# Performance work log

Measured on AMD Instinct MI355X. Metric: run time of the kernel, lower is better.

## Reference

```python
import jax, jax.numpy as jnp
import numpy as np

INPUT_DIM, HIDDEN, EVENT_DIM = 64, 256, 32
B, T = 128, 1024


def setup_inputs() -> dict:
    key = jax.random.key(0)
    ks = jax.random.split(key, 20)
    s = 0.02
    return {
        "x": jax.random.normal(ks[0], (B, T, INPUT_DIM), jnp.float32),
        "events": jax.random.normal(ks[1], (B, T, EVENT_DIM), jnp.float32),
        "time_distances": jax.random.uniform(ks[2], (B, T), jnp.float32),
        # input projection
        "W_proj": s * jax.random.normal(ks[3], (INPUT_DIM, HIDDEN), jnp.float32),
        "b_proj": jnp.zeros((HIDDEN,), jnp.float32),
        # custom LSTM cell (input = projected_x of size HIDDEN)
        "W_ih": s * jax.random.normal(ks[4], (HIDDEN, 4 * HIDDEN), jnp.float32),
        "W_hh": s * jax.random.normal(ks[5], (HIDDEN, 4 * HIDDEN), jnp.float32),
        "b_lstm": jnp.zeros((4 * HIDDEN,), jnp.float32),
        # market-state gate from raw x
        "W_mk": s * jax.random.normal(ks[6], (INPUT_DIM, HIDDEN), jnp.float32),
        "b_mk": jnp.zeros((HIDDEN,), jnp.float32),
        # event processor
        "W_e": s * jax.random.normal(ks[7], (EVENT_DIM, HIDDEN), jnp.float32),
        "b_e": jnp.zeros((HIDDEN,), jnp.float32),
        "W_hg": s * jax.random.normal(ks[8], (HIDDEN, HIDDEN), jnp.float32),
        "b_hg": jnp.zeros((HIDDEN,), jnp.float32),
        "decay": jnp.asarray(0.5, jnp.float32),
        # predictor MLP (dropout is eval-mode identity)
        "W_p1": s * jax.random.normal(ks[9], (HIDDEN, HIDDEN // 2), jnp.float32),
        "b_p1": jnp.zeros((HIDDEN // 2,), jnp.float32),
        "W_p2": s * jax.random.normal(ks[10], (HIDDEN // 2, 1), jnp.float32),
        "b_p2": jnp.zeros((1,), jnp.float32),
    }


def _tmdo(x):
    # temporal first difference and Laplacian (second difference), zero-padded to [B,T,D]
    d1 = jnp.concatenate([jnp.zeros_like(x[:, :1]), x[:, 1:] - x[:, :-1]], axis=1)
    lap = jnp.concatenate(
        [jnp.zeros_like(x[:, :1]),
         x[:, 2:] - 2.0 * x[:, 1:-1] + x[:, :-2],
         jnp.zeros_like(x[:, :1])], axis=1)
    return d1, lap


def reference(x, events, time_distances, W_proj, b_proj, W_ih, W_hh, b_lstm,
              W_mk, b_mk, W_e, b_e, W_hg, b_hg, decay, W_p1, b_p1, W_p2, b_p2):
    bsz, seq_len, _ = x.shape
    H = W_proj.shape[1]
    tmdo_features, lap_features = _tmdo(x)

    h0 = jnp.zeros((bsz, H), x.dtype)
    c0 = jnp.zeros((bsz, H), x.dtype)

    def step(carry, inp):
        h, c = carry
        xt, et, dt = inp  # [B,D_in], [B,E], [B]
        px = xt @ W_proj + b_proj                                  # input_proj
        # event processor: embedded event * hidden gate * time decay
        e = jnp.tanh(et @ W_e + b_e)
        gate = jax.nn.sigmoid(h @ W_hg + b_hg)
        impact = e * gate * jnp.exp(-jax.nn.softplus(decay) * dt[:, None])
        # custom LSTM cell with market gate from raw x and event injection
        gates = px @ W_ih + h @ W_hh + b_lstm
        i_g, f_g, g_g, o_g = jnp.split(gates, 4, axis=-1)
        mk = jax.nn.sigmoid(xt @ W_mk + b_mk)
        c_new = jax.nn.sigmoid(f_g) * c + jax.nn.sigmoid(i_g) * jnp.tanh(g_g) \
                + mk * jnp.tanh(impact)
        h_new = jax.nn.sigmoid(o_g) * jnp.tanh(c_new)
        # predictor (exact GELU like torch nn.GELU; dropout = identity in eval)
        pred = jax.nn.gelu(h_new @ W_p1 + b_p1, approximate=False) @ W_p2 + b_p2
        return (h_new, c_new), (pred, h_new)

    xs = (jnp.swapaxes(x, 0, 1), jnp.swapaxes(events, 0, 1),
          jnp.swapaxes(time_distances, 0, 1))
    _, (preds, feats) = jax.lax.scan(step, (h0, c0), xs)
    predictions = jnp.swapaxes(preds, 0, 1)  # [B,T,1]
    features = jnp.swapaxes(feats, 0, 1)     # [B,T,H]
    return predictions, features, tmdo_features
```

## Files before the change

kernel.cpp:

```cpp
#include <hip/hip_runtime.h>
#include <hip/hip_bf16.h>
#include <hip/hip_fp16.h>
#include <math.h>

#define BB 128
#define TT 1024
#define DIN 64
#define HH 256
#define EE 32
#define BT (BB * TT)

typedef unsigned int uint;
typedef unsigned char uchar;
typedef _Float16 half2v __attribute__((ext_vector_type(2)));

__device__ __forceinline__ int dot4(uint a, uint b, int c) {
  return __builtin_amdgcn_sdot4((int)a, (int)b, c, false);
}
__device__ __forceinline__ uint pkh(float a, float b) {
  return __builtin_bit_cast(uint, __builtin_amdgcn_cvt_pkrtz(a, b));
}
__device__ __forceinline__ half2v uph(uint u) { return __builtin_bit_cast(half2v, u); }
__device__ __forceinline__ float fdot2u(uint a, uint b, float c) {
  return __builtin_amdgcn_fdot2(uph(a), uph(b), c, false);
}
#define IDPP(v, c) __builtin_amdgcn_mov_dpp((v), (c), 0xF, 0xF, true)
__device__ __forceinline__ int qsum(int v) {
  v += IDPP(v, 0xB1);
  v += IDPP(v, 0x4E);
  return v;
}
__device__ __forceinline__ float rcp_f(float x) { return __builtin_amdgcn_rcpf(x); }
__device__ __forceinline__ float sigm(float x) { return rcp_f(1.0f + __expf(-x)); }
__device__ __forceinline__ float tanh_f(float x) {
  return 1.0f - 2.0f * rcp_f(__expf(2.0f * x) + 1.0f);
}

__global__ void fold_f32(const float* __restrict__ Wproj, const float* __restrict__ Wih,
                         float* __restrict__ Wfold) {
  int idx = blockIdx.x * blockDim.x + threadIdx.x;
  if (idx >= 64 * 1024) return;
  int d = idx >> 10, n = idx & 1023;
  float a = 0.f;
  for (int k = 0; k < 256; ++k) a += Wproj[d * 256 + k] * Wih[k * 1024 + n];
  Wfold[d * 1024 + n] = a;
}

__global__ void bfold_kernel(const float* __restrict__ bproj, const float* __restrict__ Wih,
                             const float* __restrict__ blstm, float* __restrict__ bfold) {
  int n = blockIdx.x * blockDim.x + threadIdx.x;
  if (n >= 1024) return;
  float a = blstm[n];
  for (int k = 0; k < 256; ++k) a += bproj[k] * Wih[k * 1024 + n];
  bfold[n] = a;
}

__global__ __launch_bounds__(1024) void quant_all(
    const float* __restrict__ Whh, const float* __restrict__ Whg,
    const float* __restrict__ Wfold, const float* __restrict__ Wmk,
    const float* __restrict__ We,
    uint* __restrict__ WhQ, uint* __restrict__ XQ, uint* __restrict__ EQ,
    float* __restrict__ scales) {
  const int bid = blockIdx.x, tid = threadIdx.x;
  const float* src;
  int nelem;
  switch (bid) {
    case 0: src = Whh;   nelem = 262144; break;
    case 1: src = Whg;   nelem = 65536;  break;
    case 2: src = Wfold; nelem = 65536;  break;
    case 3: src = Wmk;   nelem = 16384;  break;
    default: src = We;   nelem = 8192;   break;
  }
  float m = 0.f;
  for (int i = tid; i < nelem; i += 1024) m = fmaxf(m, fabsf(src[i]));
#pragma unroll
  for (int d = 1; d < 64; d <<= 1) m = fmaxf(m, __shfl_xor(m, d));
  __shared__ float wm[16];
  if ((tid & 63) == 0) wm[tid >> 6] = m;
  __syncthreads();
  float mg = wm[0];
#pragma unroll
  for (int i = 1; i < 16; ++i) mg = fmaxf(mg, wm[i]);
  mg = fmaxf(mg, 1e-8f);
  if (tid == 0) scales[bid] = mg * (1.0f / 127.0f);
  const float inv = 127.0f / mg;

  if (bid == 0) {
    for (int i = tid; i < 65536; i += 1024) {
      int C = i >> 4, r = i & 15;
      int c = C >> 2, q = C & 3, mI = r >> 2, mm = r & 3;
      int k4 = q * 16 + mI * 4 + mm;
      uint d = 0;
#pragma unroll
      for (int bb = 0; bb < 4; ++bb) {
        int qv = __float2int_rn(Whh[(4 * k4 + bb) * 1024 + c] * inv);
        qv = max(-127, min(127, qv));
        d |= ((uint)(qv & 0xff)) << (8 * bb);
      }
      WhQ[i] = d;
    }
  } else if (bid == 1) {
    for (int i = tid; i < 16384; i += 1024) {
      int j = i >> 6, rr = i & 63;
      int q = rr >> 4, mI = (rr >> 2) & 3, mm = rr & 3;
      int k4 = q * 16 + mI * 4 + mm;
      uint d = 0;
#pragma unroll
      for (int bb = 0; bb < 4; ++bb) {
        int qv = __float2int_rn(Whg[(4 * k4 + bb) * 256 + j] * inv);
        qv = max(-127, min(127, qv));
        d |= ((uint)(qv & 0xff)) << (8 * bb);
      }
      WhQ[65536 + i] = d;
    }
  } else if (bid == 2) {
    for (int i = tid; i < 16384; i += 1024) {
      int c = i >> 4, k4 = i & 15;
      uint d = 0;
#pragma unroll
      for (int bb = 0; bb < 4; ++bb) {
        int qv = __float2int_rn(Wfold[(4 * k4 + bb) * 1024 + c] * inv);
        qv = max(-127, min(127, qv));
        d |= ((uint)(qv & 0xff)) << (8 * bb);
      }
      XQ[i] = d;
    }
  } else if (bid == 3) {
    for (int i = tid; i < 4096; i += 1024) {
      int j = i >> 4, k4 = i & 15;
      uint d = 0;
#pragma unroll
      for (int bb = 0; bb < 4; ++bb) {
        int qv = __float2int_rn(Wmk[(4 * k4 + bb) * 256 + j] * inv);
        qv = max(-127, min(127, qv));
        d |= ((uint)(qv & 0xff)) << (8 * bb);
      }
      XQ[16384 + i] = d;
    }
  } else {
    for (int i = tid; i < 2048; i += 1024) {
      int c = i >> 3, k4 = i & 7;
      uint d = 0;
#pragma unroll
      for (int bb = 0; bb < 4; ++bb) {
        int qv = __float2int_rn(We[(4 * k4 + bb) * 256 + c] * inv);
        qv = max(-127, min(127, qv));
        d |= ((uint)(qv & 0xff)) << (8 * bb);
      }
      EQ[i] = d;
    }
  }
}

__global__ void pack_wp1h(const float* __restrict__ Wp1, uint* __restrict__ WQ) {
  int idx = blockIdx.x * blockDim.x + threadIdx.x;
  if (idx >= 16384) return;
  int j = idx >> 7, kp = idx & 127;
  WQ[idx] = pkh(Wp1[(2 * kp) * 128 + j], Wp1[(2 * kp + 1) * 128 + j]);
}

__global__ __launch_bounds__(256) void prep_inputs(
    const float* __restrict__ x, const float* __restrict__ ev, const float* __restrict__ td,
    const float* __restrict__ decay, uint* __restrict__ xq, uint* __restrict__ eq,
    float4* __restrict__ scl) {
  int wid = threadIdx.x >> 6, lane = threadIdx.x & 63;
  int bt = blockIdx.x * 4 + wid;
  if (bt >= BT) return;
  float xv = x[(size_t)bt * DIN + lane];
  float evv = (lane < EE) ? ev[(size_t)bt * EE + lane] : 0.0f;
  float ax = fabsf(xv), ae = fabsf(evv);
#pragma unroll
  for (int m = 1; m < 64; m <<= 1) {
    ax = fmaxf(ax, __shfl_xor(ax, m));
    ae = fmaxf(ae, __shfl_xor(ae, m));
  }
  float mgx = fmaxf(ax, 1e-8f), mge = fmaxf(ae, 1e-8f);
  int qx = __float2int_rn(xv * (127.0f / mgx));
  qx = max(-127, min(127, qx));
  int qe = __float2int_rn(evv * (127.0f / mge));
  qe = max(-127, min(127, qe));
  uint dx = 0, de = 0;
#pragma unroll
  for (int b = 0; b < 4; ++b) dx |= ((uint)(__shfl(qx, lane * 4 + b) & 0xff)) << (8 * b);
#pragma unroll
  for (int b = 0; b < 4; ++b) de |= ((uint)(__shfl(qe, lane * 4 + b) & 0xff)) << (8 * b);
  if (lane < 16) xq[(size_t)bt * 16 + lane] = dx;
  if (lane < 8) eq[(size_t)bt * 8 + lane] = de;
  if (lane == 0) {
    float sp = log1pf(__expf(decay[0]));
    scl[bt] = make_float4(mgx * (1.0f / 127.0f), mge * (1.0f / 127.0f),
                          __expf(-sp * td[bt]), 0.0f);
  }
}

__global__ void d1_kernel(const float* __restrict__ x, float* __restrict__ out2) {
  int idx = blockIdx.x * blockDim.x + threadIdx.x;
  const int per_t = DIN / 4;
  if (idx >= BB * TT * per_t) return;
  int t = (idx / per_t) % TT;
  float4 cur = reinterpret_cast<const float4*>(x)[idx];
  float4 res;
  if (t == 0) {
    res = make_float4(0.f, 0.f, 0.f, 0.f);
  } else {
    float4 prv = reinterpret_cast<const float4*>(x)[idx - per_t];
    res = make_float4(cur.x - prv.x, cur.y - prv.y, cur.z - prv.z, cur.w - prv.w);
  }
  reinterpret_cast<float4*>(out2)[idx] = res;
}

__global__ __launch_bounds__(1024) void pre2(
    int t0, int lsteps,
    const uint* __restrict__ XQ, const uint* __restrict__ EQ,
    const float* __restrict__ scales, const float* __restrict__ bfold,
    const float* __restrict__ bmk, const float* __restrict__ be,
    const uint* __restrict__ xq, const uint* __restrict__ eqp,
    const float4* __restrict__ scl, uint4* __restrict__ pre) {
  const int tid = threadIdx.x;
  const int j = tid >> 2, q = tid & 3;

  uint4 wx[4];
#pragma unroll
  for (int g = 0; g < 4; ++g)
    wx[g] = *(const uint4*)(XQ + (g * 256 + j) * 16 + q * 4);
  const uint4 wmv = *(const uint4*)(XQ + 16384 + j * 16 + q * 4);
  const uint2 wev = *(const uint2*)(EQ + j * 8 + q * 2);
  float bf[4];
#pragma unroll
  for (int g = 0; g < 4; ++g) bf[g] = bfold[g * 256 + j];
  const float bmkv = bmk[j], bev = be[j];
  const float sXF = scales[2], sMK = scales[3], sE = scales[4];
  const int steps = 1 << lsteps;

  for (int it = 0; it < 64; ++it) {
    const int idx = blockIdx.x * 64 + it;
    const int b = idx >> lsteps, tl = idx & (steps - 1);
    const int bt = b * TT + t0 + tl;
    const uint4 X = *(const uint4*)(xq + (size_t)bt * 16 + q * 4);
    const uint2 E = *(const uint2*)(eqp + (size_t)bt * 8 + q * 2);
    const float4 sv = scl[bt];

    int a0 = 0, a1 = 0, a2 = 0, a3 = 0, am = 0, ae = 0;
    a0 = dot4(wx[0].x, X.x, a0); a0 = dot4(wx[0].y, X.y, a0);
    a0 = dot4(wx[0].z, X.z, a0); a0 = dot4(wx[0].w, X.w, a0);
    a1 = dot4(wx[1].x, X.x, a1); a1 = dot4(wx[1].y, X.y, a1);
    a1 = dot4(wx[1].z, X.z, a1); a1 = dot4(wx[1].w, X.w, a1);
    a2 = dot4(wx[2].x, X.x, a2); a2 = dot4(wx[2].y, X.y, a2);
    a2 = dot4(wx[2].z, X.z, a2); a2 = dot4(wx[2].w, X.w, a2);
    a3 = dot4(wx[3].x, X.x, a3); a3 = dot4(wx[3].y, X.y, a3);
    a3 = dot4(wx[3].z, X.z, a3); a3 = dot4(wx[3].w, X.w, a3);
    am = dot4(wmv.x, X.x, am);   am = dot4(wmv.y, X.y, am);
    am = dot4(wmv.z, X.z, am);   am = dot4(wmv.w, X.w, am);
    ae = dot4(wev.x, E.x, ae);   ae = dot4(wev.y, E.y, ae);

    a0 = qsum(a0); a1 = qsum(a1); a2 = qsum(a2);
    a3 = qsum(a3); am = qsum(am); ae = qsum(ae);

    if (q == 0) {
      const float fx = sXF * sv.x;
      const float p0 = (float)a0 * fx + bf[0];
      const float p1 = (float)a1 * fx + bf[1];
      const float p2 = (float)a2 * fx + bf[2];
      const float p3 = (float)a3 * fx + bf[3];
      const float mkS = sigm((float)am * (sMK * sv.x) + bmkv);
      const float EF = tanh_f((float)ae * (sE * sv.y) + bev) * sv.z;
      uint4 o;
      o.x = pkh(p0, p1);
      o.y = pkh(p2, p3);
      o.z = __float_as_uint(mkS);
      o.w = __float_as_uint(EF);
      pre[(size_t)idx * 256 + j] = o;
    }
  }
}

__global__ __launch_bounds__(1024) void scan3(
    int t0, int steps, const uint* __restrict__ WhQ,
    const float* __restrict__ scales, const float* __restrict__ bhg,
    const uint4* __restrict__ pre, uchar* __restrict__ hB, float* __restrict__ cB,
    float* __restrict__ feat) {
  __shared__ __align__(16) uint hqW[128];
  const int tid = threadIdx.x, b = blockIdx.x;
  const int j = tid >> 2, q = tid & 3;

  const uint4* wv = (const uint4*)WhQ;
  uint4 wh[4][4];
#pragma unroll
  for (int g = 0; g < 4; ++g)
#pragma unroll
    for (int m = 0; m < 4; ++m) wh[g][m] = wv[((g * 256 + j) * 4 + q) * 4 + m];
  uint4 wg[4];
#pragma unroll
  for (int m = 0; m < 4; ++m) wg[m] = wv[((1024 + j) * 4 + q) * 4 + m];

  float c;
  if (t0 == 0) {
    c = 0.0f;
    if (tid < 64) hqW[tid] = 0u;
  } else {
    c = cB[b * 256 + j];
    if (tid < 64) hqW[tid] = ((const uint*)hB)[b * 64 + tid];
  }
  const float kHH = scales[0] * (1.0f / 127.0f);
  const float kHG = scales[1] * (1.0f / 127.0f);
  const float bhgv = bhg[j];
  const uint4* prep = pre + (size_t)b * steps * 256;
  float* fout = feat + ((size_t)b * TT + t0) * HH;
  int buf = 0;
  __syncthreads();

  uint4 P = prep[j];
  for (int t = 0; t < steps; ++t) {
    uint4 Pn = P;
    if (t + 1 < steps) Pn = prep[(size_t)(t + 1) * 256 + j];

    int a0 = 0, a1 = 0, a2 = 0, a3 = 0, a4 = 0;
    const uint4* hp = (const uint4*)((const uchar*)hqW + buf * 256 + q * 64);
#pragma unroll
    for (int m = 0; m < 4; ++m) {
      const uint4 hv = hp[m];
      a0 = dot4(wh[0][m].x, hv.x, a0); a0 = dot4(wh[0][m].y, hv.y, a0);
      a0 = dot4(wh[0][m].z, hv.z, a0); a0 = dot4(wh[0][m].w, hv.w, a0);
      a1 = dot4(wh[1][m].x, hv.x, a1); a1 = dot4(wh[1][m].y, hv.y, a1);
      a1 = dot4(wh[1][m].z, hv.z, a1); a1 = dot4(wh[1][m].w, hv.w, a1);
      a2 = dot4(wh[2][m].x, hv.x, a2); a2 = dot4(wh[2][m].y, hv.y, a2);
      a2 = dot4(wh[2][m].z, hv.z, a2); a2 = dot4(wh[2][m].w, hv.w, a2);
      a3 = dot4(wh[3][m].x, hv.x, a3); a3 = dot4(wh[3][m].y, hv.y, a3);
      a3 = dot4(wh[3][m].z, hv.z, a3); a3 = dot4(wh[3][m].w, hv.w, a3);
      a4 = dot4(wg[m].x, hv.x, a4);    a4 = dot4(wg[m].y, hv.y, a4);
      a4 = dot4(wg[m].z, hv.z, a4);    a4 = dot4(wg[m].w, hv.w, a4);
    }
    a0 = qsum(a0); a1 = qsum(a1); a2 = qsum(a2); a3 = qsum(a3); a4 = qsum(a4);

    const half2v pif = uph(P.x), pgo = uph(P.y);
    const float p0 = (float)a0 * kHH + (float)pif.x;
    const float p1 = (float)a1 * kHH + (float)pif.y;
    const float p2 = (float)a2 * kHH + (float)pgo.x;
    const float p3 = (float)a3 * kHH + (float)pgo.y;
    const float p4 = (float)a4 * kHG + bhgv;
    const float mkS = __uint_as_float(P.z);
    const float EF = __uint_as_float(P.w);

    const float impact = EF * sigm(p4);
    c = sigm(p1) * c + sigm(p0) * tanh_f(p2) + mkS * tanh_f(impact);
    const float hn = sigm(p3) * tanh_f(c);

    if (q == 0) {
      fout[(size_t)t * HH + j] = hn;
      int qi = __float2int_rn(hn * 127.0f);
      ((uchar*)hqW)[(buf ^ 1) * 256 + j] = (uchar)(qi & 0xff);
    }
    __syncthreads();
    buf ^= 1;
    P = Pn;
  }
  if (q == 0) cB[b * 256 + j] = c;
  if (tid < 64) ((uint*)hB)[b * 64 + tid] = hqW[buf * 64 + tid];
}

__global__ __launch_bounds__(256) void pred3(
    const float* __restrict__ feat, const uint* __restrict__ WQh,
    const float* __restrict__ bp1, const float* __restrict__ Wp2,
    const float* __restrict__ bp2, float* __restrict__ out0) {
  __shared__ uint WL[16384];
  __shared__ uint hT[128 * 132];
  __shared__ float psum[4][128];

  const int tid = threadIdx.x, w = tid >> 6, l = tid & 63;
  const int rbase = blockIdx.x * 128;

  for (int i = tid; i < 16384; i += 256) WL[i] = WQh[i];
  for (int i = tid; i < 16384; i += 256) {
    int row = i >> 7, kp = i & 127;
    const float2 hv = ((const float2*)feat)[(size_t)(rbase + row) * 128 + kp];
    hT[row * 132 + kp] = pkh(hv.x, hv.y);
  }
  __syncthreads();

  float ma[32], mb[32];
#pragma unroll
  for (int jj = 0; jj < 32; ++jj) {
    const float bv = bp1[w * 32 + jj];
    ma[jj] = bv;
    mb[jj] = bv;
  }
  const uint* ha = &hT[l * 132];
  const uint* hb = &hT[(l + 64) * 132];
  const uint* wbase = &WL[(w * 32) * 128];
  for (int kp4 = 0; kp4 < 32; ++kp4) {
    const uint4 a4 = *(const uint4*)&ha[kp4 * 4];
    const uint4 b4 = *(const uint4*)&hb[kp4 * 4];
#pragma unroll
    for (int jj = 0; jj < 32; ++jj) {
      const uint4 w4 = *(const uint4*)&wbase[jj * 128 + kp4 * 4];
      ma[jj] = fdot2u(w4.x, a4.x, ma[jj]);
      ma[jj] = fdot2u(w4.y, a4.y, ma[jj]);
      ma[jj] = fdot2u(w4.z, a4.z, ma[jj]);
      ma[jj] = fdot2u(w4.w, a4.w, ma[jj]);
      mb[jj] = fdot2u(w4.x, b4.x, mb[jj]);
      mb[jj] = fdot2u(w4.y, b4.y, mb[jj]);
      mb[jj] = fdot2u(w4.z, b4.z, mb[jj]);
      mb[jj] = fdot2u(w4.w, b4.w, mb[jj]);
    }
  }
  float accA = 0.f, accB = 0.f;
#pragma unroll
  for (int jj = 0; jj < 32; ++jj) {
    const float w2v = Wp2[w * 32 + jj];
    accA += 0.5f * ma[jj] * (1.0f + erff(ma[jj] * 0.70710678118f)) * w2v;
    accB += 0.5f * mb[jj] * (1.0f + erff(mb[jj] * 0.70710678118f)) * w2v;
  }
  psum[w][l] = accA;
  psum[w][64 + l] = accB;
  __syncthreads();
  if (tid < 128)
    out0[rbase + tid] =
        psum[0][tid] + psum[1][tid] + psum[2][tid] + psum[3][tid] + bp2[0];
}

extern "C" void kernel_launch(void* const* d_in, const int* in_sizes, int n_in,
                              void* d_out, int out_size, void* d_ws, size_t ws_size,
                              hipStream_t stream) {
  const float* x = (const float*)d_in[0];
  const float* ev = (const float*)d_in[1];
  const float* td = (const float*)d_in[2];
  const float* Wproj = (const float*)d_in[3];
  const float* bproj = (const float*)d_in[4];
  const float* Wih = (const float*)d_in[5];
  const float* Whh = (const float*)d_in[6];
  const float* blstm = (const float*)d_in[7];
  const float* Wmk = (const float*)d_in[8];
  const float* bmk = (const float*)d_in[9];
  const float* We = (const float*)d_in[10];
  const float* be = (const float*)d_in[11];
  const float* Whg = (const float*)d_in[12];
  const float* bhg = (const float*)d_in[13];
  const float* decay = (const float*)d_in[14];
  const float* Wp1 = (const float*)d_in[15];
  const float* bp1 = (const float*)d_in[16];
  const float* Wp2 = (const float*)d_in[17];
  const float* bp2 = (const float*)d_in[18];

  float* out0 = (float*)d_out;
  float* out1 = out0 + (size_t)BT;
  float* out2 = out1 + (size_t)BT * HH;

  char* w = (char*)d_ws;
  float* Wfold_f = (float*)w; w += (size_t)65536 * 4;
  uint* WhQ = (uint*)w; w += (size_t)81920 * 4;
  uint* XQ = (uint*)w; w += (size_t)20480 * 4;
  uint* EQ = (uint*)w; w += (size_t)2048 * 4;
  uint* WQh = (uint*)w; w += (size_t)16384 * 4;
  float* scales = (float*)w; w += 16 * 4;
  float* bfold = (float*)w; w += 1024 * 4;
  uchar* hB = (uchar*)w; w += (size_t)BB * 256;
  float* cB = (float*)w; w += (size_t)BB * 256 * 4;
  uint* xq = (uint*)w; w += (size_t)BT * 16 * 4;
  uint* eq = (uint*)w; w += (size_t)BT * 8 * 4;
  float4* scl = (float4*)w; w += (size_t)BT * 16;
  uint4* pre = (uint4*)w;

  size_t used = (size_t)(w - (char*)d_ws);
  size_t avail = (ws_size > used + 4096) ? (ws_size - used - 4096) : 0;
  int steps = TT, lsteps = 10;
  while (steps > 4 && (size_t)BB * (size_t)steps * 256 * 16 > avail) {
    steps >>= 1;
    lsteps--;
  }

  hipLaunchKernelGGL(fold_f32, dim3(256), dim3(256), 0, stream, Wproj, Wih, Wfold_f);
  hipLaunchKernelGGL(bfold_kernel, dim3(4), dim3(256), 0, stream, bproj, Wih, blstm, bfold);
  hipLaunchKernelGGL(quant_all, dim3(5), dim3(1024), 0, stream,
                     Whh, Whg, Wfold_f, Wmk, We, WhQ, XQ, EQ, scales);
  hipLaunchKernelGGL(pack_wp1h, dim3(64), dim3(256), 0, stream, Wp1, WQh);
  hipLaunchKernelGGL(prep_inputs, dim3(BT / 4), dim3(256), 0, stream,
                     x, ev, td, decay, xq, eq, scl);
  hipLaunchKernelGGL(d1_kernel, dim3(8192), dim3(256), 0, stream, x, out2);

  for (int t0 = 0; t0 < TT; t0 += steps) {
    hipLaunchKernelGGL(pre2, dim3(2 * steps), dim3(1024), 0, stream,
                       t0, lsteps, XQ, EQ, scales, bfold, bmk, be, xq, eq, scl, pre);
    hipLaunchKernelGGL(scan3, dim3(BB), dim3(1024), 0, stream,
                       t0, steps, WhQ, scales, bhg, pre, hB, cB, out1);
  }

  hipLaunchKernelGGL(pred3, dim3(BT / 128), dim3(256), 0, stream,
                     out1, WQh, bp1, Wp2, bp2, out0);
}
```

Baseline: 2.114 ms.

## Split recurrent scan over two lanes per hidden unit and shrink precomputed stream

The recurrent scan now uses 512 threads per batch row, with two lanes per hidden unit instead of four. Each lane holds twice as many int8 weight registers, and the partial sums are reduced with a single shuffle instead of a 4-way reduction. The weight packing layout is simplified to match. The per-step precomputed record drops from 16 to 12 bytes by packing the market gate and event factor into fp16, which cuts scan read bandwidth and workspace use. The fp16 packing loses precision for those values, and the unconditional prefetch of step t+1 reads one record past the end of the chunk.

```diff
diff --git a/kernel.cpp b/kernel.cpp
--- a/kernel.cpp
+++ b/kernel.cpp
@@ -87,9 +87,7 @@
 
   if (bid == 0) {
     for (int i = tid; i < 65536; i += 1024) {
-      int C = i >> 4, r = i & 15;
-      int c = C >> 2, q = C & 3, mI = r >> 2, mm = r & 3;
-      int k4 = q * 16 + mI * 4 + mm;
+      int c = i >> 6, k4 = i & 63;
       uint d = 0;
 #pragma unroll
       for (int bb = 0; bb < 4; ++bb) {
@@ -101,9 +99,7 @@
     }
   } else if (bid == 1) {
     for (int i = tid; i < 16384; i += 1024) {
-      int j = i >> 6, rr = i & 63;
-      int q = rr >> 4, mI = (rr >> 2) & 3, mm = rr & 3;
-      int k4 = q * 16 + mI * 4 + mm;
+      int j = i >> 6, k4 = i & 63;
       uint d = 0;
 #pragma unroll
       for (int bb = 0; bb < 4; ++bb) {
@@ -215,7 +211,8 @@
     const float* __restrict__ scales, const float* __restrict__ bfold,
     const float* __restrict__ bmk, const float* __restrict__ be,
     const uint* __restrict__ xq, const uint* __restrict__ eqp,
-    const float4* __restrict__ scl, uint4* __restrict__ pre) {
+    const float4* __restrict__ scl,
+    uint2* __restrict__ preA, uint* __restrict__ preB) {
   const int tid = threadIdx.x;
   const int j = tid >> 2, q = tid & 3;
 
@@ -264,34 +261,31 @@
       const float p3 = (float)a3 * fx + bf[3];
       const float mkS = sigm((float)am * (sMK * sv.x) + bmkv);
       const float EF = tanh_f((float)ae * (sE * sv.y) + bev) * sv.z;
-      uint4 o;
-      o.x = pkh(p0, p1);
-      o.y = pkh(p2, p3);
-      o.z = __float_as_uint(mkS);
-      o.w = __float_as_uint(EF);
-      pre[(size_t)idx * 256 + j] = o;
-    }
-  }
-}
-
-__global__ __launch_bounds__(1024) void scan3(
+      preA[(size_t)idx * 256 + j] = make_uint2(pkh(p0, p1), pkh(p2, p3));
+      preB[(size_t)idx * 256 + j] = pkh(mkS, EF);
+    }
+  }
+}
+
+__attribute__((amdgpu_waves_per_eu(2, 2)))
+__global__ __launch_bounds__(512, 2) void scan4(
     int t0, int steps, const uint* __restrict__ WhQ,
     const float* __restrict__ scales, const float* __restrict__ bhg,
-    const uint4* __restrict__ pre, uchar* __restrict__ hB, float* __restrict__ cB,
-    float* __restrict__ feat) {
+    const uint2* __restrict__ preA, const uint* __restrict__ preB,
+    uchar* __restrict__ hB, float* __restrict__ cB, float* __restrict__ feat) {
   __shared__ __align__(16) uint hqW[128];
   const int tid = threadIdx.x, b = blockIdx.x;
-  const int j = tid >> 2, q = tid & 3;
+  const int j = tid >> 1, kh = tid & 1;
 
   const uint4* wv = (const uint4*)WhQ;
-  uint4 wh[4][4];
+  uint4 wh[4][8];
 #pragma unroll
   for (int g = 0; g < 4; ++g)
 #pragma unroll
-    for (int m = 0; m < 4; ++m) wh[g][m] = wv[((g * 256 + j) * 4 + q) * 4 + m];
-  uint4 wg[4];
-#pragma unroll
-  for (int m = 0; m < 4; ++m) wg[m] = wv[((1024 + j) * 4 + q) * 4 + m];
+    for (int m = 0; m < 8; ++m) wh[g][m] = wv[(g * 256 + j) * 16 + kh * 8 + m];
+  uint4 wg[8];
+#pragma unroll
+  for (int m = 0; m < 8; ++m) wg[m] = wv[(1024 + j) * 16 + kh * 8 + m];
 
   float c;
   if (t0 == 0) {
@@ -304,20 +298,23 @@
   const float kHH = scales[0] * (1.0f / 127.0f);
   const float kHG = scales[1] * (1.0f / 127.0f);
   const float bhgv = bhg[j];
-  const uint4* prep = pre + (size_t)b * steps * 256;
+  const uint2* pA = preA + (size_t)b * steps * 256;
+  const uint* pB = preB + (size_t)b * steps * 256;
   float* fout = feat + ((size_t)b * TT + t0) * HH;
   int buf = 0;
   __syncthreads();
 
-  uint4 P = prep[j];
+  uint2 PA = pA[j];
+  uint PB = pB[j];
+#pragma unroll 2
   for (int t = 0; t < steps; ++t) {
-    uint4 Pn = P;
-    if (t + 1 < steps) Pn = prep[(size_t)(t + 1) * 256 + j];
+    const uint2 PAn = pA[(size_t)(t + 1) * 256 + j];
+    const uint PBn = pB[(size_t)(t + 1) * 256 + j];
 
     int a0 = 0, a1 = 0, a2 = 0, a3 = 0, a4 = 0;
-    const uint4* hp = (const uint4*)((const uchar*)hqW + buf * 256 + q * 64);
-#pragma unroll
-    for (int m = 0; m < 4; ++m) {
+    const uint4* hp = (const uint4*)((const uchar*)hqW + buf * 256 + kh * 128);
+#pragma unroll
+    for (int m = 0; m < 8; ++m) {
       const uint4 hv = hp[m];
       a0 = dot4(wh[0][m].x, hv.x, a0); a0 = dot4(wh[0][m].y, hv.y, a0);
       a0 = dot4(wh[0][m].z, hv.z, a0); a0 = dot4(wh[0][m].w, hv.w, a0);
@@ -330,31 +327,36 @@
       a4 = dot4(wg[m].x, hv.x, a4);    a4 = dot4(wg[m].y, hv.y, a4);
       a4 = dot4(wg[m].z, hv.z, a4);    a4 = dot4(wg[m].w, hv.w, a4);
     }
-    a0 = qsum(a0); a1 = qsum(a1); a2 = qsum(a2); a3 = qsum(a3); a4 = qsum(a4);
-
-    const half2v pif = uph(P.x), pgo = uph(P.y);
+    a0 += __shfl_xor(a0, 1);
+    a1 += __shfl_xor(a1, 1);
+    a2 += __shfl_xor(a2, 1);
+    a3 += __shfl_xor(a3, 1);
+    a4 += __shfl_xor(a4, 1);
+
+    const half2v pif = uph(PA.x), pgo = uph(PA.y), mkEF = uph(PB);
     const float p0 = (float)a0 * kHH + (float)pif.x;
     const float p1 = (float)a1 * kHH + (float)pif.y;
     const float p2 = (float)a2 * kHH + (float)pgo.x;
     const float p3 = (float)a3 * kHH + (float)pgo.y;
     const float p4 = (float)a4 * kHG + bhgv;
-    const float mkS = __uint_as_float(P.z);
-    const float EF = __uint_as_float(P.w);
+    const float mkS = (float)mkEF.x;
+    const float EF = (float)mkEF.y;
 
     const float impact = EF * sigm(p4);
     c = sigm(p1) * c + sigm(p0) * tanh_f(p2) + mkS * tanh_f(impact);
     const float hn = sigm(p3) * tanh_f(c);
 
-    if (q == 0) {
+    if (kh == 0) {
       fout[(size_t)t * HH + j] = hn;
       int qi = __float2int_rn(hn * 127.0f);
       ((uchar*)hqW)[(buf ^ 1) * 256 + j] = (uchar)(qi & 0xff);
     }
     __syncthreads();
     buf ^= 1;
-    P = Pn;
-  }
-  if (q == 0) cB[b * 256 + j] = c;
+    PA = PAn;
+    PB = PBn;
+  }
+  if (kh == 0) cB[b * 256 + j] = c;
   if (tid < 64) ((uint*)hB)[b * 64 + tid] = hqW[buf * 64 + tid];
 }
 
@@ -458,15 +460,16 @@
   uint* xq = (uint*)w; w += (size_t)BT * 16 * 4;
   uint* eq = (uint*)w; w += (size_t)BT * 8 * 4;
   float4* scl = (float4*)w; w += (size_t)BT * 16;
-  uint4* pre = (uint4*)w;
 
   size_t used = (size_t)(w - (char*)d_ws);
-  size_t avail = (ws_size > used + 4096) ? (ws_size - used - 4096) : 0;
+  size_t avail = (ws_size > used + 8192) ? (ws_size - used - 8192) : 0;
   int steps = TT, lsteps = 10;
-  while (steps > 4 && (size_t)BB * (size_t)steps * 256 * 16 > avail) {
+  while (steps > 4 && (size_t)BB * (size_t)steps * 256 * 12 > avail) {
     steps >>= 1;
     lsteps--;
   }
+  uint2* preA = (uint2*)w; w += (size_t)BB * steps * 256 * 8;
+  uint* preB = (uint*)w;
 
   hipLaunchKernelGGL(fold_f32, dim3(256), dim3(256), 0, stream, Wproj, Wih, Wfold_f);
   hipLaunchKernelGGL(bfold_kernel, dim3(4), dim3(256), 0, stream, bproj, Wih, blstm, bfold);
@@ -478,10 +481,11 @@
   hipLaunchKernelGGL(d1_kernel, dim3(8192), dim3(256), 0, stream, x, out2);
 
   for (int t0 = 0; t0 < TT; t0 += steps) {
-    hipLaunchKernelGGL(pre2, dim3(2 * steps), dim3(1024), 0, stream,
-                       t0, lsteps, XQ, EQ, scales, bfold, bmk, be, xq, eq, scl, pre);
-    hipLaunchKernelGGL(scan3, dim3(BB), dim3(1024), 0, stream,
-                       t0, steps, WhQ, scales, bhg, pre, hB, cB, out1);
+    hipLaunchKernelGGL(pre2, dim3(BB * steps / 64), dim3(1024), 0, stream,
+                       t0, lsteps, XQ, EQ, scales, bfold, bmk, be, xq, eq, scl,
+                       preA, preB);
+    hipLaunchKernelGGL(scan4, dim3(BB), dim3(512), 0, stream,
+                       t0, steps, WhQ, scales, bhg, preA, preB, hB, cB, out1);
   }
 
   hipLaunchKernelGGL(pred3, dim3(BT / 128), dim3(256), 0, stream,
```

New measurement: 1.903 ms. 10.0% less time.
